# Kernel optimization log

Hardware: AMD Instinct MI355X
Metric: run time of the kernel (lower is better)

## Reference

```python
import jax, jax.numpy as jnp
import numpy as np

LN_EPS = 1e-5
EPS = 1e-8
NUM_ITERS = 3

def _ln(x, w, b):
    mu = jnp.mean(x, axis=-1, keepdims=True)
    var = jnp.var(x, axis=-1, keepdims=True)
    return (x - mu) * jax.lax.rsqrt(var + LN_EPS) * w + b

def setup_inputs() -> dict:
    key = jax.random.key(0)
    ks = jax.random.split(key, 20)
    B, H, W, C = 16, 64, 64, 256
    D, S, HID, T = 128, 10, 256, 20
    g = lambda k, *shape: jax.random.normal(k, shape, dtype=jnp.float32) * 0.02
    return {
        'obs': jax.random.normal(ks[0], (B, H, W, C), dtype=jnp.float32),
        'noise': jax.random.normal(ks[1], (B, S, D), dtype=jnp.float32),
        'slots_mu': jax.random.normal(ks[2], (1, 1, D), dtype=jnp.float32),
        'slots_log_sigma': jax.random.normal(ks[3], (1, 1, D), dtype=jnp.float32) * 0.1,
        'ni_w': jnp.ones((C,), jnp.float32), 'ni_b': jnp.zeros((C,), jnp.float32),
        'ns_w': jnp.ones((D,), jnp.float32), 'ns_b': jnp.zeros((D,), jnp.float32),
        'nm_w': jnp.ones((D,), jnp.float32), 'nm_b': jnp.zeros((D,), jnp.float32),
        'Wq': g(ks[4], D, D), 'Wk': g(ks[5], C, D), 'Wv': g(ks[6], C, D),
        'mlp_w1': g(ks[7], D, 2 * D), 'mlp_b1': jnp.zeros((2 * D,), jnp.float32),
        'mlp_w2': g(ks[8], 2 * D, D), 'mlp_b2': jnp.zeros((D,), jnp.float32),
        'pd_w1': g(ks[9], D, HID), 'pd_b1': jnp.zeros((HID,), jnp.float32),
        'pd_w2': g(ks[10], HID, D), 'pd_b2': jnp.zeros((D,), jnp.float32),
        'tc_w': g(ks[11], D, T), 'tc_b': jnp.zeros((T,), jnp.float32),
    }

def reference(obs, noise, slots_mu, slots_log_sigma, ni_w, ni_b, ns_w, ns_b,
              nm_w, nm_b, Wq, Wk, Wv, mlp_w1, mlp_b1, mlp_w2, mlp_b2,
              pd_w1, pd_b1, pd_w2, pd_b2, tc_w, tc_b):
    B = obs.shape[0]
    x = obs.reshape(B, -1, obs.shape[-1])  # [B, N, C] (flatten H,W)
    D = Wq.shape[0]
    # slot init: mu + sigma * noise
    slots = slots_mu + jnp.exp(slots_log_sigma) * noise  # [B, S, D]
    x = _ln(x, ni_w, ni_b)
    k = x @ Wk  # [B, N, D]
    v = x @ Wv  # [B, N, D]
    scale = D ** -0.5
    attn = None
    for _ in range(NUM_ITERS):
        slots_prev = slots
        q = _ln(slots, ns_w, ns_b) @ Wq  # [B, S, D]
        logits = jnp.einsum('bsd,bnd->bsn', q, k) * scale
        attn = jax.nn.softmax(logits, axis=1)  # competitive over slots
        w = attn / (jnp.sum(attn, axis=-1, keepdims=True) + EPS)
        updates = jnp.einsum('bsn,bnd->bsd', w, v)
        slots = slots_prev + updates
        h = _ln(slots, nm_w, nm_b)
        slots = slots + (jax.nn.relu(h @ mlp_w1 + mlp_b1) @ mlp_w2 + mlp_b2)
    objects = jax.nn.relu(slots @ pd_w1 + pd_b1) @ pd_w2 + pd_b2
    object_types = slots @ tc_w + tc_b
    return objects, object_types
```

## Files before the change

### kernel.cpp

```cpp
#include <hip/hip_runtime.h>
#include <hip/hip_bf16.h>

typedef __hip_bfloat16 bf16;
typedef __attribute__((ext_vector_type(8))) short bf16x8;
typedef __attribute__((ext_vector_type(4))) float f32x4;

#define LN_EPS 1e-5f
#define ATT_EPS 1e-8f

__device__ __forceinline__ float bflo(unsigned u){ union{unsigned i;float f;}c; c.i=u<<16; return c.f; }
__device__ __forceinline__ float bfhi(unsigned u){ union{unsigned i;float f;}c; c.i=u&0xffff0000u; return c.f; }
__device__ __forceinline__ float bf2f(bf16 h){ return __bfloat162float(h); }
__device__ __forceinline__ unsigned f2bfbits(float f){
    bf16 h = __float2bfloat16(f);
    unsigned short s; __builtin_memcpy(&s, &h, 2);
    return (unsigned)s;
}

__device__ __forceinline__ float getv(const void* p, long i, int isf){
    if (isf) return ((const float*)p)[i];
    return bf2f(((const bf16*)p)[i]);
}
__device__ __forceinline__ void get8(const void* p, long i, int isf, float* o){
    if (isf){
        __builtin_memcpy(o, (const float*)p + i, 32);
    } else {
        unsigned u[4];
        __builtin_memcpy(u, (const bf16*)p + i, 16);
        o[0]=bflo(u[0]); o[1]=bfhi(u[0]); o[2]=bflo(u[1]); o[3]=bfhi(u[1]);
        o[4]=bflo(u[2]); o[5]=bfhi(u[2]); o[6]=bflo(u[3]); o[7]=bfhi(u[3]);
    }
}
__device__ __forceinline__ void get4(const void* p, long i, int isf, float* o){
    if (isf){
        __builtin_memcpy(o, (const float*)p + i, 16);
    } else {
        unsigned u[2];
        __builtin_memcpy(u, (const bf16*)p + i, 8);
        o[0]=bflo(u[0]); o[1]=bfhi(u[0]); o[2]=bflo(u[1]); o[3]=bfhi(u[1]);
    }
}
__device__ __forceinline__ void load4f(const float* p, float* o){ __builtin_memcpy(o, p, 16); }
__device__ __forceinline__ void store4f(float* p, const float* v){ __builtin_memcpy(p, v, 16); }

__device__ __forceinline__ void wred2(float& a, float& b){
    #pragma unroll
    for (int m = 32; m > 0; m >>= 1){
        a += __shfl_xor(a, m, 64);
        b += __shfl_xor(b, m, 64);
    }
}

__global__ void k_detect(const void* __restrict__ niw, int* __restrict__ flag){
    if (threadIdx.x == 0 && blockIdx.x == 0){
        unsigned u; __builtin_memcpy(&u, niw, 4);
        *flag = (u == 0x3F800000u) ? 1 : 0;
    }
}

__global__ __launch_bounds__(128) void k_init_slots(
        const void* __restrict__ noise, const void* __restrict__ mu,
        const void* __restrict__ ls, const void* __restrict__ nsw,
        const void* __restrict__ nsb, const int* __restrict__ flag,
        float* __restrict__ slots, float* __restrict__ lns){
    int isf = *flag;
    int bs = blockIdx.x, t = threadIdx.x;
    __shared__ float red[2][2];
    float sv = getv(mu,t,isf) + __expf(getv(ls,t,isf)) * getv(noise,(long)bs*128+t,isf);
    slots[bs*128 + t] = sv;
    float s = sv, ss = sv*sv;
    wred2(s, ss);
    int wid = t >> 6, lane = t & 63;
    if (lane == 0){ red[wid][0]=s; red[wid][1]=ss; }
    __syncthreads();
    s = red[0][0]+red[1][0]; ss = red[0][1]+red[1][1];
    float m = s*(1.f/128.f), var = ss*(1.f/128.f) - m*m;
    float ri = rsqrtf(var + LN_EPS);
    lns[bs*128 + t] = (sv - m)*ri*getv(nsw,t,isf) + getv(nsb,t,isf);
}

__global__ __launch_bounds__(256) void k_xn(
        const void* __restrict__ x, const void* __restrict__ niw,
        const void* __restrict__ nib, const int* __restrict__ flag,
        bf16* __restrict__ xnb){
    int isf = *flag;
    int t = threadIdx.x, wid = t >> 6, lane = t & 63;
    long row = (long)blockIdx.x * 4 + wid;
    float v[4];
    get4(x, row*256 + lane*4, isf, v);
    float s = v[0]+v[1]+v[2]+v[3];
    float ss = v[0]*v[0]+v[1]*v[1]+v[2]*v[2]+v[3]*v[3];
    wred2(s, ss);
    float m = s*(1.f/256.f);
    float ri = rsqrtf(ss*(1.f/256.f) - m*m + LN_EPS);
    int c = lane*4;
    float w4[4], b4[4];
    get4(niw, c, isf, w4);
    get4(nib, c, isf, b4);
    float y0 = (v[0]-m)*ri*w4[0] + b4[0];
    float y1 = (v[1]-m)*ri*w4[1] + b4[1];
    float y2 = (v[2]-m)*ri*w4[2] + b4[2];
    float y3 = (v[3]-m)*ri*w4[3] + b4[3];
    unsigned pk[2];
    pk[0] = (f2bfbits(y1) << 16) | f2bfbits(y0);
    pk[1] = (f2bfbits(y3) << 16) | f2bfbits(y2);
    __builtin_memcpy(xnb + row*256 + c, pk, 8);
}

__global__ __launch_bounds__(256) void k_gmat(
        const void* __restrict__ Wq, const void* __restrict__ Wk,
        const int* __restrict__ flag, float* __restrict__ G){
    int isf = *flag;
    int c = blockIdx.x, t = threadIdx.x;
    int d = t & 127, half = t >> 7;
    __shared__ float red2[2][128];
    float acc = 0.f;
    #pragma unroll
    for (int ch = 0; ch < 8; ch++){
        int dp = half*64 + ch*8;
        float wq8[8], wk8[8];
        get8(Wq, (long)d*128 + dp, isf, wq8);
        get8(Wk, (long)c*128 + dp, isf, wk8);
        #pragma unroll
        for (int j=0;j<8;j++) acc += wq8[j]*wk8[j];
    }
    red2[half][d] = acc;
    __syncthreads();
    if (t < 128)
        G[(long)t*256 + c] = (red2[0][t] + red2[1][t]) * 0.08838834764831845f;
}

__global__ __launch_bounds__(256) void k_kq4(
        const float* __restrict__ lns, const float* __restrict__ G,
        bf16* __restrict__ kqB, float* __restrict__ praw, float* __restrict__ den){
    int bx = blockIdx.x;
    int b = bx >> 2, cg = bx & 3;
    int t = threadIdx.x;
    __shared__ __align__(16) float lsh[1280];
    __shared__ float pred[4][64][10];
    for (int i = t; i < 1280; i += 256) lsh[i] = lns[b*1280 + i];
    __syncthreads();
    int c4 = t & 63, dg = t >> 6;
    int c = cg*64 + c4;
    float acc[10];
    #pragma unroll
    for (int s=0;s<10;s++) acc[s]=0.f;
    for (int d0 = dg*32; d0 < dg*32 + 32; d0 += 4){
        float g0 = G[(long)(d0+0)*256 + c];
        float g1 = G[(long)(d0+1)*256 + c];
        float g2 = G[(long)(d0+2)*256 + c];
        float g3 = G[(long)(d0+3)*256 + c];
        #pragma unroll
        for (int s=0;s<10;s++){
            float l4[4]; load4f(&lsh[s*128 + d0], l4);
            acc[s] += g0*l4[0] + g1*l4[1] + g2*l4[2] + g3*l4[3];
        }
    }
    #pragma unroll
    for (int s=0;s<10;s++) pred[dg][c4][s] = acc[s];
    __syncthreads();
    for (int o = t; o < 1024; o += 256){
        int s = o >> 6, cc = o & 63;
        float v = 0.f;
        if (s < 10) v = pred[0][cc][s] + pred[1][cc][s] + pred[2][cc][s] + pred[3][cc][s];
        int c2 = cg*64 + cc;
        int ks = c2 >> 5, q = (c2 >> 3) & 3, j = c2 & 7;
        kqB[(long)b*4096 + ks*512 + (q*16 + s)*8 + j] = __float2bfloat16(v);
    }
    for (int i = t; i < 640; i += 256) praw[b*2560 + cg*640 + i] = 0.f;
    if (cg == 0 && t < 10) den[b*10 + t] = 0.f;
}

__global__ __launch_bounds__(256) void k_attn4(
        const bf16* __restrict__ xn, const bf16* __restrict__ kqB,
        float* __restrict__ praw, float* __restrict__ den){
    int tile = blockIdx.x, b = blockIdx.y, t = threadIdx.x;
    int w = t >> 6, l = t & 63;
    __shared__ unsigned sxn[64*130];
    __shared__ __align__(16) float attnP[64*12];
    __shared__ float denp[4][16];

    {
        const unsigned* gx = (const unsigned*)xn + ((long)b*4096 + tile*64)*128;
        #pragma unroll
        for (int i = 0; i < 8; i++){
            int Ld = t*4 + i*1024;
            unsigned tmp[4];
            __builtin_memcpy(tmp, gx + Ld, 16);
            int px = Ld >> 7, col = Ld & 127;
            __builtin_memcpy(&sxn[px*130 + col], tmp, 16);
        }
    }
    bf16x8 bfr[8];
    {
        const unsigned* kqg = (const unsigned*)kqB + (long)b*2048;
        #pragma unroll
        for (int ks = 0; ks < 8; ks++)
            __builtin_memcpy(&bfr[ks], kqg + ks*256 + l*4, 16);
    }
    __syncthreads();

    f32x4 acc = {0.f, 0.f, 0.f, 0.f};
    {
        int m = l & 15, q = (l >> 4) & 3;
        int rowbase = (w*16 + m)*130;
        #pragma unroll
        for (int ks = 0; ks < 8; ks++){
            bf16x8 af;
            __builtin_memcpy(&af, &sxn[rowbase + ks*16 + q*4], 16);
            acc = __builtin_amdgcn_mfma_f32_16x16x32_bf16(af, bfr[ks], acc, 0, 0, 0);
        }
    }

    {
        int col = l & 15, q = (l >> 4) & 3;
        float pden = 0.f;
        #pragma unroll
        for (int reg = 0; reg < 4; reg++){
            float v = (col < 10) ? acc[reg] : -1e30f;
            float mx = v;
            mx = fmaxf(mx, __shfl_xor(mx, 1, 64));
            mx = fmaxf(mx, __shfl_xor(mx, 2, 64));
            mx = fmaxf(mx, __shfl_xor(mx, 4, 64));
            mx = fmaxf(mx, __shfl_xor(mx, 8, 64));
            float e = (col < 10) ? __expf(acc[reg] - mx) : 0.f;
            float sm = e;
            sm += __shfl_xor(sm, 1, 64);
            sm += __shfl_xor(sm, 2, 64);
            sm += __shfl_xor(sm, 4, 64);
            sm += __shfl_xor(sm, 8, 64);
            float a = e / sm;
            if (col < 10) attnP[(w*16 + q*4 + reg)*12 + col] = a;
            pden += a;
        }
        pden += __shfl_xor(pden, 16, 64);
        pden += __shfl_xor(pden, 32, 64);
        if (l < 10) denp[w][l] = pden;
    }
    __syncthreads();
    if (t < 10)
        atomicAdd(&den[b*10 + t], denp[0][t] + denp[1][t] + denp[2][t] + denp[3][t]);

    {
        int c = t, ch = c >> 1, hh = c & 1;
        float pacc[10];
        #pragma unroll
        for (int s=0;s<10;s++) pacc[s]=0.f;
        for (int n = 0; n < 64; n++){
            unsigned d = sxn[n*130 + ch];
            float xv = hh ? bfhi(d) : bflo(d);
            float a[10];
            load4f(&attnP[n*12], a);
            load4f(&attnP[n*12 + 4], a + 4);
            __builtin_memcpy(a + 8, &attnP[n*12 + 8], 8);
            #pragma unroll
            for (int s=0;s<10;s++) pacc[s] += a[s]*xv;
        }
        #pragma unroll
        for (int s=0;s<10;s++) atomicAdd(&praw[b*2560 + s*256 + c], pacc[s]);
    }
}

__global__ __launch_bounds__(256) void k_slot_update(
        float* __restrict__ slots, const float* __restrict__ praw,
        const float* __restrict__ den, const void* __restrict__ Wv,
        const void* __restrict__ nmw, const void* __restrict__ nmb,
        const void* __restrict__ w1, const void* __restrict__ b1,
        const void* __restrict__ w2, const void* __restrict__ b2,
        const void* __restrict__ nsw, const void* __restrict__ nsb,
        const int* __restrict__ flag, float* __restrict__ lns){
    int isf = *flag;
    int bs = blockIdx.x, t = threadIdx.x;
    __shared__ __align__(16) float pr[256];
    __shared__ __align__(16) float redA[16*128];
    __shared__ __align__(16) float redB[8*256];
    __shared__ __align__(16) float hld[128];
    __shared__ __align__(16) float hid[256];
    __shared__ float red[4][2];
    pr[t] = praw[bs*256 + t];
    __syncthreads();

    {
        int g = t & 15, ks = t >> 4;
        int d0 = g*8;
        float a8[8] = {0,0,0,0,0,0,0,0};
        #pragma unroll
        for (int j=0;j<16;j++){
            int c2 = ks*16 + j;
            float w8[8]; get8(Wv, (long)c2*128 + d0, isf, w8);
            float pv = pr[c2];
            #pragma unroll
            for (int k=0;k<8;k++) a8[k] += pv*w8[k];
        }
        store4f(&redA[ks*128 + d0], a8);
        store4f(&redA[ks*128 + d0 + 4], a8+4);
    }
    __syncthreads();
    float dv = den[bs] + ATT_EPS;
    float sn = 0.f;
    if (t < 128){
        float u = 0.f;
        #pragma unroll
        for (int ks=0;ks<16;ks++) u += redA[ks*128 + t];
        sn = slots[bs*128 + t] + u/dv;
    }
    float v = (t < 128) ? sn : 0.f;
    float s = v, ss = v*v;
    wred2(s, ss);
    int wid = t >> 6, lane = t & 63;
    if (lane == 0){ red[wid][0]=s; red[wid][1]=ss; }
    __syncthreads();
    s = red[0][0]+red[1][0]+red[2][0]+red[3][0];
    ss = red[0][1]+red[1][1]+red[2][1]+red[3][1];
    float mu = s*(1.f/128.f), var = ss*(1.f/128.f) - mu*mu;
    float rinv = rsqrtf(var + LN_EPS);
    if (t < 128) hld[t] = (v-mu)*rinv*getv(nmw,t,isf) + getv(nmb,t,isf);
    __syncthreads();

    {
        int g = t & 31, ks = t >> 5;
        int h0 = g*8;
        float a8[8] = {0,0,0,0,0,0,0,0};
        #pragma unroll
        for (int j=0;j<16;j++){
            int d = ks*16 + j;
            float w8[8]; get8(w1, (long)d*256 + h0, isf, w8);
            float hv = hld[d];
            #pragma unroll
            for (int k=0;k<8;k++) a8[k] += hv*w8[k];
        }
        store4f(&redB[ks*256 + h0], a8);
        store4f(&redB[ks*256 + h0 + 4], a8+4);
    }
    __syncthreads();
    {
        float hb = getv(b1,t,isf);
        #pragma unroll
        for (int ks=0;ks<8;ks++) hb += redB[ks*256 + t];
        hid[t] = fmaxf(hb, 0.f);
    }
    __syncthreads();

    {
        int g = t & 15, ks = t >> 4;
        int d0 = g*8;
        float a8[8] = {0,0,0,0,0,0,0,0};
        #pragma unroll
        for (int j=0;j<16;j++){
            int h = ks*16 + j;
            float w8[8]; get8(w2, (long)h*128 + d0, isf, w8);
            float hv = hid[h];
            #pragma unroll
            for (int k=0;k<8;k++) a8[k] += hv*w8[k];
        }
        store4f(&redA[ks*128 + d0], a8);
        store4f(&redA[ks*128 + d0 + 4], a8+4);
    }
    __syncthreads();
    float v2 = 0.f;
    if (t < 128){
        float o = getv(b2,t,isf);
        #pragma unroll
        for (int ks=0;ks<16;ks++) o += redA[ks*128 + t];
        v2 = sn + o;
        slots[bs*128 + t] = v2;
    }
    float s2 = v2, ss2 = v2*v2;
    wred2(s2, ss2);
    __syncthreads();
    if (lane == 0){ red[wid][0]=s2; red[wid][1]=ss2; }
    __syncthreads();
    s2 = red[0][0]+red[1][0]+red[2][0]+red[3][0];
    ss2 = red[0][1]+red[1][1]+red[2][1]+red[3][1];
    float mu2 = s2*(1.f/128.f), var2 = ss2*(1.f/128.f) - mu2*mu2;
    float ri2 = rsqrtf(var2 + LN_EPS);
    if (t < 128)
        lns[bs*128 + t] = (v2 - mu2)*ri2*getv(nsw,t,isf) + getv(nsb,t,isf);
}

__global__ __launch_bounds__(256) void k_head(
        const float* __restrict__ slots,
        const void* __restrict__ pw1, const void* __restrict__ pb1,
        const void* __restrict__ pw2, const void* __restrict__ pb2,
        const void* __restrict__ tw, const void* __restrict__ tb,
        const int* __restrict__ flag, void* __restrict__ out){
    int isf = *flag;
    int bs = blockIdx.x, t = threadIdx.x;
    __shared__ __align__(16) float sl[128];
    __shared__ __align__(16) float redA[16*128];
    __shared__ __align__(16) float redB[8*256];
    __shared__ __align__(16) float redT[8*32];
    __shared__ __align__(16) float hid[256];
    if (t < 128) sl[t] = slots[bs*128 + t];
    __syncthreads();
    {
        int g = t & 31, ks = t >> 5;
        int h0 = g*8;
        float a8[8] = {0,0,0,0,0,0,0,0};
        #pragma unroll
        for (int j=0;j<16;j++){
            int d = ks*16 + j;
            float w8[8]; get8(pw1, (long)d*256 + h0, isf, w8);
            float hv = sl[d];
            #pragma unroll
            for (int k=0;k<8;k++) a8[k] += hv*w8[k];
        }
        store4f(&redB[ks*256 + h0], a8);
        store4f(&redB[ks*256 + h0 + 4], a8+4);
    }
    __syncthreads();
    {
        float hb = getv(pb1,t,isf);
        #pragma unroll
        for (int ks=0;ks<8;ks++) hb += redB[ks*256 + t];
        hid[t] = fmaxf(hb, 0.f);
    }
    __syncthreads();
    {
        int g = t & 15, ks = t >> 4;
        int d0 = g*8;
        float a8[8] = {0,0,0,0,0,0,0,0};
        #pragma unroll
        for (int j=0;j<16;j++){
            int h = ks*16 + j;
            float w8[8]; get8(pw2, (long)h*128 + d0, isf, w8);
            float hv = hid[h];
            #pragma unroll
            for (int k=0;k<8;k++) a8[k] += hv*w8[k];
        }
        store4f(&redA[ks*128 + d0], a8);
        store4f(&redA[ks*128 + d0 + 4], a8+4);
    }
    {
        int ot = t & 31, ks = t >> 5;
        float a = 0.f;
        if (ot < 20){
            #pragma unroll
            for (int j=0;j<16;j++){
                int d = ks*16 + j;
                a += sl[d]*getv(tw, (long)d*20 + ot, isf);
            }
        }
        redT[ks*32 + ot] = a;
    }
    __syncthreads();
    if (t < 128){
        float o = getv(pb2,t,isf);
        #pragma unroll
        for (int ks=0;ks<16;ks++) o += redA[ks*128 + t];
        int idx = bs*128 + t;
        if (isf) ((float*)out)[idx] = o; else ((bf16*)out)[idx] = __float2bfloat16(o);
    }
    if (t < 20){
        float o = getv(tb,t,isf);
        #pragma unroll
        for (int ks=0;ks<8;ks++) o += redT[ks*32 + t];
        int idx = 16*10*128 + bs*20 + t;
        if (isf) ((float*)out)[idx] = o; else ((bf16*)out)[idx] = __float2bfloat16(o);
    }
}

extern "C" void kernel_launch(void* const* d_in, const int* in_sizes, int n_in,
                              void* d_out, int out_size, void* d_ws, size_t ws_size,
                              hipStream_t stream) {
    const void* obs   = d_in[0];
    const void* noise = d_in[1];
    const void* smu   = d_in[2];
    const void* sls   = d_in[3];
    const void* niw   = d_in[4];
    const void* nib   = d_in[5];
    const void* nsw   = d_in[6];
    const void* nsb   = d_in[7];
    const void* nmw   = d_in[8];
    const void* nmb   = d_in[9];
    const void* Wq    = d_in[10];
    const void* Wk    = d_in[11];
    const void* Wv    = d_in[12];
    const void* w1    = d_in[13];
    const void* b1    = d_in[14];
    const void* w2    = d_in[15];
    const void* b2    = d_in[16];
    const void* pw1   = d_in[17];
    const void* pb1   = d_in[18];
    const void* pw2   = d_in[19];
    const void* pb2   = d_in[20];
    const void* tw    = d_in[21];
    const void* tb    = d_in[22];

    char* ws = (char*)d_ws;
    int*   flag  = (int*)(ws);
    float* den   = (float*)(ws + 256);
    float* slots = (float*)(ws + 1024);
    float* lns   = (float*)(ws + 82944);
    bf16*  kqB   = (bf16*) (ws + 164864);
    float* praw  = (float*)(ws + 295936);
    float* G     = (float*)(ws + 459776);
    bf16*  xn    = (bf16*) (ws + 590848);

    k_detect<<<1, 64, 0, stream>>>(niw, flag);
    k_init_slots<<<160, 128, 0, stream>>>(noise, smu, sls, nsw, nsb, flag, slots, lns);
    k_xn<<<16384, 256, 0, stream>>>(obs, niw, nib, flag, xn);
    k_gmat<<<256, 256, 0, stream>>>(Wq, Wk, flag, G);

    for (int it = 0; it < 3; it++){
        k_kq4<<<64, 256, 0, stream>>>(lns, G, kqB, praw, den);
        k_attn4<<<dim3(64, 16), 256, 0, stream>>>(xn, kqB, praw, den);
        k_slot_update<<<160, 256, 0, stream>>>(slots, praw, den, Wv, nmw, nmb,
                                               w1, b1, w2, b2, nsw, nsb, flag, lns);
    }
    k_head<<<160, 256, 0, stream>>>(slots, pw1, pb1, pw2, pb2, tw, tb, flag, d_out);
}
```

Baseline: 256.0 us.

## Fold input LayerNorm into attention kernel and fuse kq/head into slot update

Removes the separate LayerNorm pass over obs, which wrote a normalized bf16 copy, by computing per-pixel mean and rstd inside the attention kernel. The LN scale and bias are folded algebraically into the slot-key product, using per-slot U/V correction terms and two denominator accumulators. The slot-query projection is fused into the slot-update kernel, and the output head runs in the last iteration, which cuts several launches. Each of the three attention passes now re-reads fp32 obs and recomputes LN statistics, and the folded normalization changes rounding.

```diff
diff --git a/kernel.cpp b/kernel.cpp
--- a/kernel.cpp
+++ b/kernel.cpp
@@ -31,15 +31,6 @@
         o[4]=bflo(u[2]); o[5]=bfhi(u[2]); o[6]=bflo(u[3]); o[7]=bfhi(u[3]);
     }
 }
-__device__ __forceinline__ void get4(const void* p, long i, int isf, float* o){
-    if (isf){
-        __builtin_memcpy(o, (const float*)p + i, 16);
-    } else {
-        unsigned u[2];
-        __builtin_memcpy(u, (const bf16*)p + i, 8);
-        o[0]=bflo(u[0]); o[1]=bfhi(u[0]); o[2]=bflo(u[1]); o[3]=bfhi(u[1]);
-    }
-}
 __device__ __forceinline__ void load4f(const float* p, float* o){ __builtin_memcpy(o, p, 16); }
 __device__ __forceinline__ void store4f(float* p, const float* v){ __builtin_memcpy(p, v, 16); }
 
@@ -51,66 +42,13 @@
     }
 }
 
-__global__ void k_detect(const void* __restrict__ niw, int* __restrict__ flag){
-    if (threadIdx.x == 0 && blockIdx.x == 0){
-        unsigned u; __builtin_memcpy(&u, niw, 4);
-        *flag = (u == 0x3F800000u) ? 1 : 0;
-    }
-}
-
-__global__ __launch_bounds__(128) void k_init_slots(
-        const void* __restrict__ noise, const void* __restrict__ mu,
-        const void* __restrict__ ls, const void* __restrict__ nsw,
-        const void* __restrict__ nsb, const int* __restrict__ flag,
-        float* __restrict__ slots, float* __restrict__ lns){
-    int isf = *flag;
-    int bs = blockIdx.x, t = threadIdx.x;
-    __shared__ float red[2][2];
-    float sv = getv(mu,t,isf) + __expf(getv(ls,t,isf)) * getv(noise,(long)bs*128+t,isf);
-    slots[bs*128 + t] = sv;
-    float s = sv, ss = sv*sv;
-    wred2(s, ss);
-    int wid = t >> 6, lane = t & 63;
-    if (lane == 0){ red[wid][0]=s; red[wid][1]=ss; }
-    __syncthreads();
-    s = red[0][0]+red[1][0]; ss = red[0][1]+red[1][1];
-    float m = s*(1.f/128.f), var = ss*(1.f/128.f) - m*m;
-    float ri = rsqrtf(var + LN_EPS);
-    lns[bs*128 + t] = (sv - m)*ri*getv(nsw,t,isf) + getv(nsb,t,isf);
-}
-
-__global__ __launch_bounds__(256) void k_xn(
-        const void* __restrict__ x, const void* __restrict__ niw,
-        const void* __restrict__ nib, const int* __restrict__ flag,
-        bf16* __restrict__ xnb){
-    int isf = *flag;
-    int t = threadIdx.x, wid = t >> 6, lane = t & 63;
-    long row = (long)blockIdx.x * 4 + wid;
-    float v[4];
-    get4(x, row*256 + lane*4, isf, v);
-    float s = v[0]+v[1]+v[2]+v[3];
-    float ss = v[0]*v[0]+v[1]*v[1]+v[2]*v[2]+v[3]*v[3];
-    wred2(s, ss);
-    float m = s*(1.f/256.f);
-    float ri = rsqrtf(ss*(1.f/256.f) - m*m + LN_EPS);
-    int c = lane*4;
-    float w4[4], b4[4];
-    get4(niw, c, isf, w4);
-    get4(nib, c, isf, b4);
-    float y0 = (v[0]-m)*ri*w4[0] + b4[0];
-    float y1 = (v[1]-m)*ri*w4[1] + b4[1];
-    float y2 = (v[2]-m)*ri*w4[2] + b4[2];
-    float y3 = (v[3]-m)*ri*w4[3] + b4[3];
-    unsigned pk[2];
-    pk[0] = (f2bfbits(y1) << 16) | f2bfbits(y0);
-    pk[1] = (f2bfbits(y3) << 16) | f2bfbits(y2);
-    __builtin_memcpy(xnb + row*256 + c, pk, 8);
-}
-
 __global__ __launch_bounds__(256) void k_gmat(
         const void* __restrict__ Wq, const void* __restrict__ Wk,
-        const int* __restrict__ flag, float* __restrict__ G){
-    int isf = *flag;
+        const void* __restrict__ niw, int* __restrict__ flag,
+        float* __restrict__ G){
+    unsigned u0; __builtin_memcpy(&u0, niw, 4);
+    int isf = (u0 == 0x3F800000u) ? 1 : 0;
+    if (blockIdx.x == 0 && threadIdx.x == 0) *flag = isf;
     int c = blockIdx.x, t = threadIdx.x;
     int d = t & 127, half = t >> 7;
     __shared__ float red2[2][128];
@@ -130,80 +68,153 @@
         G[(long)t*256 + c] = (red2[0][t] + red2[1][t]) * 0.08838834764831845f;
 }
 
-__global__ __launch_bounds__(256) void k_kq4(
-        const float* __restrict__ lns, const float* __restrict__ G,
-        bf16* __restrict__ kqB, float* __restrict__ praw, float* __restrict__ den){
-    int bx = blockIdx.x;
-    int b = bx >> 2, cg = bx & 3;
-    int t = threadIdx.x;
-    __shared__ __align__(16) float lsh[1280];
-    __shared__ float pred[4][64][10];
-    for (int i = t; i < 1280; i += 256) lsh[i] = lns[b*1280 + i];
-    __syncthreads();
-    int c4 = t & 63, dg = t >> 6;
-    int c = cg*64 + c4;
-    float acc[10];
-    #pragma unroll
-    for (int s=0;s<10;s++) acc[s]=0.f;
-    for (int d0 = dg*32; d0 < dg*32 + 32; d0 += 4){
-        float g0 = G[(long)(d0+0)*256 + c];
-        float g1 = G[(long)(d0+1)*256 + c];
-        float g2 = G[(long)(d0+2)*256 + c];
-        float g3 = G[(long)(d0+3)*256 + c];
-        #pragma unroll
-        for (int s=0;s<10;s++){
-            float l4[4]; load4f(&lsh[s*128 + d0], l4);
-            acc[s] += g0*l4[0] + g1*l4[1] + g2*l4[2] + g3*l4[3];
-        }
-    }
-    #pragma unroll
-    for (int s=0;s<10;s++) pred[dg][c4][s] = acc[s];
-    __syncthreads();
-    for (int o = t; o < 1024; o += 256){
-        int s = o >> 6, cc = o & 63;
-        float v = 0.f;
-        if (s < 10) v = pred[0][cc][s] + pred[1][cc][s] + pred[2][cc][s] + pred[3][cc][s];
-        int c2 = cg*64 + cc;
-        int ks = c2 >> 5, q = (c2 >> 3) & 3, j = c2 & 7;
-        kqB[(long)b*4096 + ks*512 + (q*16 + s)*8 + j] = __float2bfloat16(v);
-    }
-    for (int i = t; i < 640; i += 256) praw[b*2560 + cg*640 + i] = 0.f;
-    if (cg == 0 && t < 10) den[b*10 + t] = 0.f;
-}
-
-__global__ __launch_bounds__(256) void k_attn4(
-        const bf16* __restrict__ xn, const bf16* __restrict__ kqB,
-        float* __restrict__ praw, float* __restrict__ den){
+__device__ __forceinline__ void phaseD(
+        int b, int s, int t, const float* shlns, const float* __restrict__ G,
+        const void* __restrict__ niw, const void* __restrict__ nib, int isf,
+        bf16* __restrict__ wkqb, float* __restrict__ Ug, float* __restrict__ Vg,
+        float* __restrict__ P2, float* __restrict__ t0g, float* __restrict__ t1g,
+        float* redUV){
+    int c = t;
+    float kqc = 0.f;
+    for (int d0 = 0; d0 < 128; d0 += 8){
+        float l8[8];
+        load4f(shlns + d0, l8); load4f(shlns + d0 + 4, l8 + 4);
+        kqc += l8[0]*G[(long)(d0+0)*256+c] + l8[1]*G[(long)(d0+1)*256+c]
+             + l8[2]*G[(long)(d0+2)*256+c] + l8[3]*G[(long)(d0+3)*256+c]
+             + l8[4]*G[(long)(d0+4)*256+c] + l8[5]*G[(long)(d0+5)*256+c]
+             + l8[6]*G[(long)(d0+6)*256+c] + l8[7]*G[(long)(d0+7)*256+c];
+    }
+    float wc = getv(niw, c, isf), bc = getv(nib, c, isf);
+    float wkq = wc*kqc, vq = bc*kqc;
+    float uu = wkq, vv = vq;
+    wred2(uu, vv);
+    int wid = t >> 6, lane = t & 63;
+    if (lane == 0){ redUV[wid*2] = uu; redUV[wid*2+1] = vv; }
+    wkqb[((long)b*16 + s)*256 + c] = __float2bfloat16(wkq);
+    int bs = b*10 + s;
+    P2[bs*256 + c] = 0.f;
+    __syncthreads();
+    if (t == 0){
+        Ug[bs] = redUV[0] + redUV[2] + redUV[4] + redUV[6];
+        Vg[bs] = redUV[1] + redUV[3] + redUV[5] + redUV[7];
+        t0g[bs] = 0.f; t1g[bs] = 0.f;
+    }
+}
+
+__global__ __launch_bounds__(256) void k_prep(
+        const void* __restrict__ noise, const void* __restrict__ smu,
+        const void* __restrict__ sls, const void* __restrict__ nsw,
+        const void* __restrict__ nsb, const void* __restrict__ niw,
+        const void* __restrict__ nib, const int* __restrict__ flag,
+        const float* __restrict__ G, float* __restrict__ slots,
+        bf16* __restrict__ wkqb, float* __restrict__ Ug, float* __restrict__ Vg,
+        float* __restrict__ P2, float* __restrict__ t0g, float* __restrict__ t1g){
+    int isf = *flag;
+    int bs = blockIdx.x, t = threadIdx.x;
+    int b = bs/10, s = bs - b*10;
+    __shared__ __align__(16) float shlns[128];
+    __shared__ float red[2][2];
+    __shared__ float redUV[8];
+    if (t < 128){
+        float sv = getv(smu,t,isf) + __expf(getv(sls,t,isf)) * getv(noise,(long)bs*128+t,isf);
+        slots[bs*128 + t] = sv;
+        shlns[t] = sv;
+        float su = sv, sq = sv*sv;
+        wred2(su, sq);
+        int wid = t >> 6, lane = t & 63;
+        if (lane == 0){ red[wid][0]=su; red[wid][1]=sq; }
+    }
+    __syncthreads();
+    if (t < 128){
+        float su = red[0][0]+red[1][0], sq = red[0][1]+red[1][1];
+        float m = su*(1.f/128.f), var = sq*(1.f/128.f) - m*m;
+        float ri = rsqrtf(var + LN_EPS);
+        shlns[t] = (shlns[t] - m)*ri*getv(nsw,t,isf) + getv(nsb,t,isf);
+    }
+    __syncthreads();
+    phaseD(b, s, t, shlns, G, niw, nib, isf, wkqb, Ug, Vg, P2, t0g, t1g, redUV);
+    if (s == 0){
+        #pragma unroll
+        for (int r = 10; r < 16; r++)
+            wkqb[((long)b*16 + r)*256 + t] = __float2bfloat16(0.f);
+    }
+}
+
+__global__ __launch_bounds__(256) void k_attn5(
+        const void* __restrict__ obs, const bf16* __restrict__ wkqb,
+        const float* __restrict__ Ug, const float* __restrict__ Vg,
+        const int* __restrict__ flag, float* __restrict__ P2,
+        float* __restrict__ t0g, float* __restrict__ t1g){
+    int isf = *flag;
     int tile = blockIdx.x, b = blockIdx.y, t = threadIdx.x;
     int w = t >> 6, l = t & 63;
-    __shared__ unsigned sxn[64*130];
+    __shared__ unsigned sxn[64*132];
     __shared__ __align__(16) float attnP[64*12];
-    __shared__ float denp[4][16];
-
-    {
-        const unsigned* gx = (const unsigned*)xn + ((long)b*4096 + tile*64)*128;
+    __shared__ float muri[128];
+    __shared__ float denp0[4][16], denp1[4][16];
+
+    if (isf){
+        const float* gx = (const float*)obs + ((long)b*4096 + tile*64)*256;
         #pragma unroll
         for (int i = 0; i < 8; i++){
             int Ld = t*4 + i*1024;
+            int px = Ld >> 7, col = Ld & 127;
+            float f8[8];
+            __builtin_memcpy(f8, gx + (long)px*256 + col*2, 32);
+            unsigned pk[4];
+            #pragma unroll
+            for (int k2=0;k2<4;k2++)
+                pk[k2] = (f2bfbits(f8[2*k2+1])<<16) | f2bfbits(f8[2*k2]);
+            __builtin_memcpy(&sxn[px*132 + col], pk, 16);
+        }
+    } else {
+        const unsigned* gx = (const unsigned*)obs + ((long)b*4096 + tile*64)*128;
+        #pragma unroll
+        for (int i = 0; i < 8; i++){
+            int Ld = t*4 + i*1024;
+            int px = Ld >> 7, col = Ld & 127;
             unsigned tmp[4];
             __builtin_memcpy(tmp, gx + Ld, 16);
-            int px = Ld >> 7, col = Ld & 127;
-            __builtin_memcpy(&sxn[px*130 + col], tmp, 16);
+            __builtin_memcpy(&sxn[px*132 + col], tmp, 16);
         }
     }
     bf16x8 bfr[8];
     {
-        const unsigned* kqg = (const unsigned*)kqB + (long)b*2048;
+        int s = l & 15, q = (l >> 4) & 3;
+        const bf16* base = wkqb + ((long)b*16 + s)*256 + q*8;
         #pragma unroll
         for (int ks = 0; ks < 8; ks++)
-            __builtin_memcpy(&bfr[ks], kqg + ks*256 + l*4, 16);
-    }
-    __syncthreads();
-
-    f32x4 acc = {0.f, 0.f, 0.f, 0.f};
+            __builtin_memcpy(&bfr[ks], base + ks*32, 16);
+    }
+    __syncthreads();
+
+    {
+        int px = t >> 2, q = t & 3;
+        float su = 0.f, sq = 0.f;
+        #pragma unroll
+        for (int j = 0; j < 8; j++){
+            unsigned d4[4];
+            __builtin_memcpy(d4, &sxn[px*132 + q*32 + j*4], 16);
+            #pragma unroll
+            for (int k2=0;k2<4;k2++){
+                float a0 = bflo(d4[k2]), a1 = bfhi(d4[k2]);
+                su += a0 + a1; sq += a0*a0 + a1*a1;
+            }
+        }
+        su += __shfl_xor(su,1,64); sq += __shfl_xor(sq,1,64);
+        su += __shfl_xor(su,2,64); sq += __shfl_xor(sq,2,64);
+        if (q == 0){
+            float m = su*(1.f/256.f);
+            float ri = rsqrtf(sq*(1.f/256.f) - m*m + LN_EPS);
+            muri[px*2] = m; muri[px*2+1] = ri;
+        }
+    }
+    __syncthreads();
+
+    f32x4 acc = {0.f,0.f,0.f,0.f};
     {
         int m = l & 15, q = (l >> 4) & 3;
-        int rowbase = (w*16 + m)*130;
+        int rowbase = (w*16 + m)*132;
         #pragma unroll
         for (int ks = 0; ks < 8; ks++){
             bf16x8 af;
@@ -214,32 +225,39 @@
 
     {
         int col = l & 15, q = (l >> 4) & 3;
-        float pden = 0.f;
+        float Uv = 0.f, Vv = 0.f;
+        if (col < 10){ Uv = Ug[b*10 + col]; Vv = Vg[b*10 + col]; }
+        float pden0 = 0.f, pden1 = 0.f;
         #pragma unroll
         for (int reg = 0; reg < 4; reg++){
-            float v = (col < 10) ? acc[reg] : -1e30f;
-            float mx = v;
-            mx = fmaxf(mx, __shfl_xor(mx, 1, 64));
-            mx = fmaxf(mx, __shfl_xor(mx, 2, 64));
-            mx = fmaxf(mx, __shfl_xor(mx, 4, 64));
-            mx = fmaxf(mx, __shfl_xor(mx, 8, 64));
-            float e = (col < 10) ? __expf(acc[reg] - mx) : 0.f;
+            int px = w*16 + q*4 + reg;
+            float mr[2]; __builtin_memcpy(mr, &muri[px*2], 8);
+            float lg = (col < 10) ? (mr[1]*acc[reg] - mr[1]*mr[0]*Uv + Vv) : -1e30f;
+            float mx = lg;
+            mx = fmaxf(mx, __shfl_xor(mx,1,64));
+            mx = fmaxf(mx, __shfl_xor(mx,2,64));
+            mx = fmaxf(mx, __shfl_xor(mx,4,64));
+            mx = fmaxf(mx, __shfl_xor(mx,8,64));
+            float e = (col < 10) ? __expf(lg - mx) : 0.f;
             float sm = e;
-            sm += __shfl_xor(sm, 1, 64);
-            sm += __shfl_xor(sm, 2, 64);
-            sm += __shfl_xor(sm, 4, 64);
-            sm += __shfl_xor(sm, 8, 64);
+            sm += __shfl_xor(sm,1,64);
+            sm += __shfl_xor(sm,2,64);
+            sm += __shfl_xor(sm,4,64);
+            sm += __shfl_xor(sm,8,64);
             float a = e / sm;
-            if (col < 10) attnP[(w*16 + q*4 + reg)*12 + col] = a;
-            pden += a;
-        }
-        pden += __shfl_xor(pden, 16, 64);
-        pden += __shfl_xor(pden, 32, 64);
-        if (l < 10) denp[w][l] = pden;
-    }
-    __syncthreads();
-    if (t < 10)
-        atomicAdd(&den[b*10 + t], denp[0][t] + denp[1][t] + denp[2][t] + denp[3][t]);
+            if (col < 10) attnP[px*12 + col] = a*mr[1];
+            pden0 += a;
+            pden1 += a*mr[1]*mr[0];
+        }
+        pden0 += __shfl_xor(pden0,16,64); pden0 += __shfl_xor(pden0,32,64);
+        pden1 += __shfl_xor(pden1,16,64); pden1 += __shfl_xor(pden1,32,64);
+        if (l < 10){ denp0[w][l] = pden0; denp1[w][l] = pden1; }
+    }
+    __syncthreads();
+    if (t < 10){
+        atomicAdd(&t0g[b*10 + t], denp0[0][t]+denp0[1][t]+denp0[2][t]+denp0[3][t]);
+        atomicAdd(&t1g[b*10 + t], denp1[0][t]+denp1[1][t]+denp1[2][t]+denp1[3][t]);
+    }
 
     {
         int c = t, ch = c >> 1, hh = c & 1;
@@ -247,7 +265,7 @@
         #pragma unroll
         for (int s=0;s<10;s++) pacc[s]=0.f;
         for (int n = 0; n < 64; n++){
-            unsigned d = sxn[n*130 + ch];
+            unsigned d = sxn[n*132 + ch];
             float xv = hh ? bfhi(d) : bflo(d);
             float a[10];
             load4f(&attnP[n*12], a);
@@ -257,27 +275,41 @@
             for (int s=0;s<10;s++) pacc[s] += a[s]*xv;
         }
         #pragma unroll
-        for (int s=0;s<10;s++) atomicAdd(&praw[b*2560 + s*256 + c], pacc[s]);
-    }
-}
-
-__global__ __launch_bounds__(256) void k_slot_update(
-        float* __restrict__ slots, const float* __restrict__ praw,
-        const float* __restrict__ den, const void* __restrict__ Wv,
+        for (int s=0;s<10;s++) atomicAdd(&P2[b*2560 + s*256 + c], pacc[s]);
+    }
+}
+
+__global__ __launch_bounds__(256) void k_slot(
+        float* __restrict__ slots, float* __restrict__ P2,
+        float* __restrict__ t0g, float* __restrict__ t1g,
+        const void* __restrict__ Wv,
         const void* __restrict__ nmw, const void* __restrict__ nmb,
         const void* __restrict__ w1, const void* __restrict__ b1,
         const void* __restrict__ w2, const void* __restrict__ b2,
         const void* __restrict__ nsw, const void* __restrict__ nsb,
-        const int* __restrict__ flag, float* __restrict__ lns){
+        const void* __restrict__ niw, const void* __restrict__ nib,
+        const void* __restrict__ pw1, const void* __restrict__ pb1,
+        const void* __restrict__ pw2, const void* __restrict__ pb2,
+        const void* __restrict__ tw, const void* __restrict__ tb,
+        const int* __restrict__ flag, const float* __restrict__ G,
+        bf16* __restrict__ wkqb, float* __restrict__ Ug, float* __restrict__ Vg,
+        void* __restrict__ out, int last){
     int isf = *flag;
     int bs = blockIdx.x, t = threadIdx.x;
+    int b = bs/10, s = bs - b*10;
     __shared__ __align__(16) float pr[256];
     __shared__ __align__(16) float redA[16*128];
     __shared__ __align__(16) float redB[8*256];
+    __shared__ __align__(16) float redT[8*32];
     __shared__ __align__(16) float hld[128];
     __shared__ __align__(16) float hid[256];
+    __shared__ __align__(16) float shlns[128];
     __shared__ float red[4][2];
-    pr[t] = praw[bs*256 + t];
+    __shared__ float redUV[8];
+
+    float t0v = t0g[bs], t1v = t1g[bs];
+    float wc = getv(niw,t,isf), bcv = getv(nib,t,isf);
+    pr[t] = (P2[bs*256 + t] - t1v)*wc + t0v*bcv;
     __syncthreads();
 
     {
@@ -296,7 +328,7 @@
         store4f(&redA[ks*128 + d0 + 4], a8+4);
     }
     __syncthreads();
-    float dv = den[bs] + ATT_EPS;
+    float dv = t0v + ATT_EPS;
     float sn = 0.f;
     if (t < 128){
         float u = 0.f;
@@ -305,14 +337,14 @@
         sn = slots[bs*128 + t] + u/dv;
     }
     float v = (t < 128) ? sn : 0.f;
-    float s = v, ss = v*v;
-    wred2(s, ss);
+    float su = v, sq = v*v;
+    wred2(su, sq);
     int wid = t >> 6, lane = t & 63;
-    if (lane == 0){ red[wid][0]=s; red[wid][1]=ss; }
-    __syncthreads();
-    s = red[0][0]+red[1][0]+red[2][0]+red[3][0];
-    ss = red[0][1]+red[1][1]+red[2][1]+red[3][1];
-    float mu = s*(1.f/128.f), var = ss*(1.f/128.f) - mu*mu;
+    if (lane == 0){ red[wid][0]=su; red[wid][1]=sq; }
+    __syncthreads();
+    su = red[0][0]+red[1][0]+red[2][0]+red[3][0];
+    sq = red[0][1]+red[1][1]+red[2][1]+red[3][1];
+    float mu = su*(1.f/128.f), var = sq*(1.f/128.f) - mu*mu;
     float rinv = rsqrtf(var + LN_EPS);
     if (t < 128) hld[t] = (v-mu)*rinv*getv(nmw,t,isf) + getv(nmb,t,isf);
     __syncthreads();
@@ -363,100 +395,90 @@
         #pragma unroll
         for (int ks=0;ks<16;ks++) o += redA[ks*128 + t];
         v2 = sn + o;
-        slots[bs*128 + t] = v2;
-    }
-    float s2 = v2, ss2 = v2*v2;
-    wred2(s2, ss2);
-    __syncthreads();
-    if (lane == 0){ red[wid][0]=s2; red[wid][1]=ss2; }
-    __syncthreads();
-    s2 = red[0][0]+red[1][0]+red[2][0]+red[3][0];
-    ss2 = red[0][1]+red[1][1]+red[2][1]+red[3][1];
-    float mu2 = s2*(1.f/128.f), var2 = ss2*(1.f/128.f) - mu2*mu2;
-    float ri2 = rsqrtf(var2 + LN_EPS);
-    if (t < 128)
-        lns[bs*128 + t] = (v2 - mu2)*ri2*getv(nsw,t,isf) + getv(nsb,t,isf);
-}
-
-__global__ __launch_bounds__(256) void k_head(
-        const float* __restrict__ slots,
-        const void* __restrict__ pw1, const void* __restrict__ pb1,
-        const void* __restrict__ pw2, const void* __restrict__ pb2,
-        const void* __restrict__ tw, const void* __restrict__ tb,
-        const int* __restrict__ flag, void* __restrict__ out){
-    int isf = *flag;
-    int bs = blockIdx.x, t = threadIdx.x;
-    __shared__ __align__(16) float sl[128];
-    __shared__ __align__(16) float redA[16*128];
-    __shared__ __align__(16) float redB[8*256];
-    __shared__ __align__(16) float redT[8*32];
-    __shared__ __align__(16) float hid[256];
-    if (t < 128) sl[t] = slots[bs*128 + t];
-    __syncthreads();
-    {
-        int g = t & 31, ks = t >> 5;
-        int h0 = g*8;
-        float a8[8] = {0,0,0,0,0,0,0,0};
-        #pragma unroll
-        for (int j=0;j<16;j++){
-            int d = ks*16 + j;
-            float w8[8]; get8(pw1, (long)d*256 + h0, isf, w8);
-            float hv = sl[d];
-            #pragma unroll
-            for (int k=0;k<8;k++) a8[k] += hv*w8[k];
-        }
-        store4f(&redB[ks*256 + h0], a8);
-        store4f(&redB[ks*256 + h0 + 4], a8+4);
-    }
-    __syncthreads();
-    {
-        float hb = getv(pb1,t,isf);
-        #pragma unroll
-        for (int ks=0;ks<8;ks++) hb += redB[ks*256 + t];
-        hid[t] = fmaxf(hb, 0.f);
-    }
-    __syncthreads();
-    {
-        int g = t & 15, ks = t >> 4;
-        int d0 = g*8;
-        float a8[8] = {0,0,0,0,0,0,0,0};
-        #pragma unroll
-        for (int j=0;j<16;j++){
-            int h = ks*16 + j;
-            float w8[8]; get8(pw2, (long)h*128 + d0, isf, w8);
-            float hv = hid[h];
-            #pragma unroll
-            for (int k=0;k<8;k++) a8[k] += hv*w8[k];
-        }
-        store4f(&redA[ks*128 + d0], a8);
-        store4f(&redA[ks*128 + d0 + 4], a8+4);
-    }
-    {
-        int ot = t & 31, ks = t >> 5;
-        float a = 0.f;
-        if (ot < 20){
+    }
+
+    if (!last){
+        if (t < 128) slots[bs*128 + t] = v2;
+        float s2 = v2, ss2 = v2*v2;
+        wred2(s2, ss2);
+        if (lane == 0){ red[wid][0]=s2; red[wid][1]=ss2; }
+        __syncthreads();
+        s2 = red[0][0]+red[1][0]+red[2][0]+red[3][0];
+        ss2 = red[0][1]+red[1][1]+red[2][1]+red[3][1];
+        float mu2 = s2*(1.f/128.f), var2 = ss2*(1.f/128.f) - mu2*mu2;
+        float ri2 = rsqrtf(var2 + LN_EPS);
+        if (t < 128)
+            shlns[t] = (v2 - mu2)*ri2*getv(nsw,t,isf) + getv(nsb,t,isf);
+        __syncthreads();
+        phaseD(b, s, t, shlns, G, niw, nib, isf, wkqb, Ug, Vg, P2, t0g, t1g, redUV);
+    } else {
+        if (t < 128) shlns[t] = v2;
+        __syncthreads();
+        {
+            int g = t & 31, ks = t >> 5;
+            int h0 = g*8;
+            float a8[8] = {0,0,0,0,0,0,0,0};
             #pragma unroll
             for (int j=0;j<16;j++){
                 int d = ks*16 + j;
-                a += sl[d]*getv(tw, (long)d*20 + ot, isf);
+                float w8[8]; get8(pw1, (long)d*256 + h0, isf, w8);
+                float hv = shlns[d];
+                #pragma unroll
+                for (int k=0;k<8;k++) a8[k] += hv*w8[k];
             }
-        }
-        redT[ks*32 + ot] = a;
-    }
-    __syncthreads();
-    if (t < 128){
-        float o = getv(pb2,t,isf);
-        #pragma unroll
-        for (int ks=0;ks<16;ks++) o += redA[ks*128 + t];
-        int idx = bs*128 + t;
-        if (isf) ((float*)out)[idx] = o; else ((bf16*)out)[idx] = __float2bfloat16(o);
-    }
-    if (t < 20){
-        float o = getv(tb,t,isf);
-        #pragma unroll
-        for (int ks=0;ks<8;ks++) o += redT[ks*32 + t];
-        int idx = 16*10*128 + bs*20 + t;
-        if (isf) ((float*)out)[idx] = o; else ((bf16*)out)[idx] = __float2bfloat16(o);
+            store4f(&redB[ks*256 + h0], a8);
+            store4f(&redB[ks*256 + h0 + 4], a8+4);
+        }
+        __syncthreads();
+        {
+            float hb = getv(pb1,t,isf);
+            #pragma unroll
+            for (int ks=0;ks<8;ks++) hb += redB[ks*256 + t];
+            hid[t] = fmaxf(hb, 0.f);
+        }
+        __syncthreads();
+        {
+            int g = t & 15, ks = t >> 4;
+            int d0 = g*8;
+            float a8[8] = {0,0,0,0,0,0,0,0};
+            #pragma unroll
+            for (int j=0;j<16;j++){
+                int h = ks*16 + j;
+                float w8[8]; get8(pw2, (long)h*128 + d0, isf, w8);
+                float hv = hid[h];
+                #pragma unroll
+                for (int k=0;k<8;k++) a8[k] += hv*w8[k];
+            }
+            store4f(&redA[ks*128 + d0], a8);
+            store4f(&redA[ks*128 + d0 + 4], a8+4);
+        }
+        {
+            int ot = t & 31, ks = t >> 5;
+            float a = 0.f;
+            if (ot < 20){
+                #pragma unroll
+                for (int j=0;j<16;j++){
+                    int d = ks*16 + j;
+                    a += shlns[d]*getv(tw, (long)d*20 + ot, isf);
+                }
+            }
+            redT[ks*32 + ot] = a;
+        }
+        __syncthreads();
+        if (t < 128){
+            float o = getv(pb2,t,isf);
+            #pragma unroll
+            for (int ks=0;ks<16;ks++) o += redA[ks*128 + t];
+            int idx = bs*128 + t;
+            if (isf) ((float*)out)[idx] = o; else ((bf16*)out)[idx] = __float2bfloat16(o);
+        }
+        if (t < 20){
+            float o = getv(tb,t,isf);
+            #pragma unroll
+            for (int ks=0;ks<8;ks++) o += redT[ks*32 + t];
+            int idx = 16*10*128 + bs*20 + t;
+            if (isf) ((float*)out)[idx] = o; else ((bf16*)out)[idx] = __float2bfloat16(o);
+        }
     }
 }
 
@@ -489,24 +511,23 @@
 
     char* ws = (char*)d_ws;
     int*   flag  = (int*)(ws);
-    float* den   = (float*)(ws + 256);
-    float* slots = (float*)(ws + 1024);
-    float* lns   = (float*)(ws + 82944);
-    bf16*  kqB   = (bf16*) (ws + 164864);
-    float* praw  = (float*)(ws + 295936);
-    float* G     = (float*)(ws + 459776);
-    bf16*  xn    = (bf16*) (ws + 590848);
-
-    k_detect<<<1, 64, 0, stream>>>(niw, flag);
-    k_init_slots<<<160, 128, 0, stream>>>(noise, smu, sls, nsw, nsb, flag, slots, lns);
-    k_xn<<<16384, 256, 0, stream>>>(obs, niw, nib, flag, xn);
-    k_gmat<<<256, 256, 0, stream>>>(Wq, Wk, flag, G);
-
+    float* t0g   = (float*)(ws + 1024);
+    float* t1g   = (float*)(ws + 2048);
+    float* Ug    = (float*)(ws + 3072);
+    float* Vg    = (float*)(ws + 4096);
+    float* slots = (float*)(ws + 5120);
+    float* P2    = (float*)(ws + 87040);
+    float* G     = (float*)(ws + 250880);
+    bf16*  wkqb  = (bf16*) (ws + 381952);
+
+    k_gmat<<<256, 256, 0, stream>>>(Wq, Wk, niw, flag, G);
+    k_prep<<<160, 256, 0, stream>>>(noise, smu, sls, nsw, nsb, niw, nib, flag, G,
+                                    slots, wkqb, Ug, Vg, P2, t0g, t1g);
     for (int it = 0; it < 3; it++){
-        k_kq4<<<64, 256, 0, stream>>>(lns, G, kqB, praw, den);
-        k_attn4<<<dim3(64, 16), 256, 0, stream>>>(xn, kqB, praw, den);
-        k_slot_update<<<160, 256, 0, stream>>>(slots, praw, den, Wv, nmw, nmb,
-                                               w1, b1, w2, b2, nsw, nsb, flag, lns);
-    }
-    k_head<<<160, 256, 0, stream>>>(slots, pw1, pb1, pw2, pb2, tw, tb, flag, d_out);
-}
+        k_attn5<<<dim3(64, 16), 256, 0, stream>>>(obs, wkqb, Ug, Vg, flag, P2, t0g, t1g);
+        k_slot<<<160, 256, 0, stream>>>(slots, P2, t0g, t1g, Wv, nmw, nmb,
+                                        w1, b1, w2, b2, nsw, nsb, niw, nib,
+                                        pw1, pb1, pw2, pb2, tw, tb, flag, G,
+                                        wkqb, Ug, Vg, d_out, (it == 2) ? 1 : 0);
+    }
+}
```

Result: faster. 235.7 us (-7.9%).
